# Kernel optimization log

Measured on AMD Instinct MI355X. Metric: run time of the kernel, lower is better.

## Reference

```python
import jax, jax.numpy as jnp
import numpy as np

EMBED_DIM = 2048
NUM_HEADS = 32
HEAD_DIM = EMBED_DIM // NUM_HEADS  # 64
SCALE = HEAD_DIM ** -0.5


def setup_inputs() -> dict:
    key = jax.random.key(0)
    k1, k2, k3, k4, k5 = jax.random.split(key, 5)
    B, S, D = 1, 2048, EMBED_DIM
    return {
        "hidden_states": jax.random.normal(k1, (B, S, D), jnp.float32),
        "w_qkv": jax.random.normal(k2, (3 * D, D), jnp.float32) * (D ** -0.5),
        "b_qkv": jax.random.normal(k3, (3 * D,), jnp.float32) * 0.02,
        "w_out": jax.random.normal(k4, (D, D), jnp.float32) * (D ** -0.5),
        "b_out": jax.random.normal(k5, (D,), jnp.float32) * 0.02,
    }


def reference(hidden_states, w_qkv, b_qkv, w_out, b_out):
    B, S, D = hidden_states.shape
    H, Hd = NUM_HEADS, HEAD_DIM
    # fused QKV projection: [B,S,3D]
    qkv = jnp.einsum("bsd,ed->bse", hidden_states, w_qkv) + b_qkv
    q, k, v = jnp.split(qkv, 3, axis=-1)
    # [B,H,S,Hd]
    q = q.reshape(B, S, H, Hd).transpose(0, 2, 1, 3)
    k = k.reshape(B, S, H, Hd).transpose(0, 2, 1, 3)
    v = v.reshape(B, S, H, Hd).transpose(0, 2, 1, 3)
    scores = jnp.einsum("bhqd,bhkd->bhqk", q, k) * SCALE
    causal = jnp.tril(jnp.ones((S, S), bool))  # [S,S]
    scores = jnp.where(causal, scores, jnp.finfo(scores.dtype).min)
    probs = jax.nn.softmax(scores, axis=-1)
    attn = jnp.einsum("bhqk,bhkd->bhqd", probs, v)
    attn = attn.transpose(0, 2, 1, 3).reshape(B, S, D)
    return jnp.einsum("bsd,ed->bse", attn, w_out) + b_out
```

## Files before the change

### kernel.cpp

```cpp
#include <hip/hip_runtime.h>
#include <hip/hip_bf16.h>

typedef __bf16 bf16;
typedef __attribute__((ext_vector_type(8))) __bf16 bf16x8;
typedef __attribute__((ext_vector_type(4))) float f32x4;

#define S_LEN 2048
#define DM 2048
#define NH 32
#define HD 64
#define QKV_LD 6144
#define SCALE2 0.18033688011112042f
#define DEFER_THR 8.0f

__device__ __forceinline__ float fast_exp2(float x) {
  return __builtin_amdgcn_exp2f(x);
}

__device__ __forceinline__ void gload_lds16(const bf16* g, const bf16* l) {
  __builtin_amdgcn_global_load_lds(
      (const __attribute__((address_space(1))) void*)(uintptr_t)g,
      (__attribute__((address_space(3))) void*)(uint32_t)(uintptr_t)l,
      16, 0, 0);
}

template <int CTRL>
__device__ __forceinline__ float fdpp(float x) {
  return __builtin_bit_cast(float,
      __builtin_amdgcn_update_dpp(0, __builtin_bit_cast(int, x), CTRL, 0xF, 0xF, true));
}
__device__ __forceinline__ float red16_max(float x) {
  x = fmaxf(x, fdpp<0xB1>(x));
  x = fmaxf(x, fdpp<0x4E>(x));
  x = fmaxf(x, fdpp<0x141>(x));
  x = fmaxf(x, fdpp<0x140>(x));
  return x;
}

__global__ __launch_bounds__(256) void cvt3_f32_bf16(
    const float* __restrict__ s0, bf16* __restrict__ d0, const int n0,
    const float* __restrict__ s1, bf16* __restrict__ d1, const int n1,
    const float* __restrict__ s2, bf16* __restrict__ d2, const int n2)
{
  const int total = n0 + n1 + n2;
  const int stride = gridDim.x * blockDim.x;
  for (int i = blockIdx.x * blockDim.x + threadIdx.x; i < total; i += stride) {
    const float* s; bf16* d; int j = i;
    if (j < n0)            { s = s0; d = d0; }
    else if (j - n0 < n1)  { s = s1; d = d1; j -= n0; }
    else                   { s = s2; d = d2; j -= n0 + n1; }
    const f32x4 a = *(const f32x4*)(s + (size_t)j * 8);
    const f32x4 b = *(const f32x4*)(s + (size_t)j * 8 + 4);
    bf16x8 r;
    r[0] = (bf16)a[0]; r[1] = (bf16)a[1]; r[2] = (bf16)a[2]; r[3] = (bf16)a[3];
    r[4] = (bf16)b[0]; r[5] = (bf16)b[1]; r[6] = (bf16)b[2]; r[7] = (bf16)b[3];
    *(bf16x8*)(d + (size_t)j * 8) = r;
  }
}

template <int BM, int BN, int WRN, int WCN, int NT, int MINW, typename TO>
__global__ __launch_bounds__(NT, MINW) void gemm_pipe(
    const bf16* __restrict__ A, const bf16* __restrict__ W,
    const float* __restrict__ bias, TO* __restrict__ C,
    const int M, const int N, const int K)
{
  constexpr int WM = BM / WRN, WN = BN / WCN;
  constexpr int MI = WM / 16, NI = WN / 16;
  constexpr int CA = (BM * 64 * 2) / (NT * 16);
  constexpr int CB = (BN * 64 * 2) / (NT * 16);
  constexpr int BUFE = (BM + BN) * 64;
  __shared__ __align__(16) bf16 lds[2 * BUFE];
  const int tid  = threadIdx.x;
  const int lane = tid & 63;
  const int wid  = tid >> 6;
  const int wr = wid / WCN, wc = wid % WCN;
  const int row0 = blockIdx.y * BM, col0 = blockIdx.x * BN;
  const int lq = lane & 15, seg = lane >> 4;

  const f32x4 fz = {0.f, 0.f, 0.f, 0.f};
  f32x4 acc[MI][NI];
#pragma unroll
  for (int i = 0; i < MI; ++i)
#pragma unroll
    for (int j = 0; j < NI; ++j) acc[i][j] = fz;

  auto stage = [&](const int kt, const int b) {
    const int k0 = kt << 6;
    bf16* Ab = lds + b * BUFE;
    bf16* Bb = Ab + BM * 64;
#pragma unroll
    for (int c = 0; c < CA; ++c) {
      const int off16 = c * NT + tid;
      const int row = off16 >> 3;
      const int ch  = (off16 & 7) ^ (row & 7);
      gload_lds16(A + (size_t)(row0 + row) * K + k0 + (ch << 3),
                  Ab + (size_t)(c * NT + (wid << 6)) * 8);
    }
#pragma unroll
    for (int c = 0; c < CB; ++c) {
      const int off16 = c * NT + tid;
      const int row = off16 >> 3;
      const int ch  = (off16 & 7) ^ (row & 7);
      gload_lds16(W + (size_t)(col0 + row) * K + k0 + (ch << 3),
                  Bb + (size_t)(c * NT + (wid << 6)) * 8);
    }
  };

  const int nt = K >> 6;
  stage(0, 0);

  for (int t = 0; t < nt; ++t) {
    asm volatile("s_waitcnt vmcnt(0)" ::: "memory");
    __builtin_amdgcn_s_barrier();
    asm volatile("" ::: "memory");
    if (t + 1 < nt) stage(t + 1, (t + 1) & 1);

    const bf16* Ab = lds + (t & 1) * BUFE;
    const bf16* Bb = Ab + BM * 64;
#pragma unroll
    for (int kk = 0; kk < 2; ++kk) {
      bf16x8 af[MI], bfr[NI];
#pragma unroll
      for (int i = 0; i < MI; ++i) {
        const int row = wr * WM + (i << 4) + lq;
        af[i] = *(const bf16x8*)(Ab + row * 64 +
                 ((((kk << 2) + seg) ^ (row & 7)) << 3));
      }
#pragma unroll
      for (int j = 0; j < NI; ++j) {
        const int row = wc * WN + (j << 4) + lq;
        bfr[j] = *(const bf16x8*)(Bb + row * 64 +
                 ((((kk << 2) + seg) ^ (row & 7)) << 3));
      }
      __builtin_amdgcn_s_setprio(1);
#pragma unroll
      for (int i = 0; i < MI; ++i)
#pragma unroll
        for (int j = 0; j < NI; ++j)
          acc[i][j] = __builtin_amdgcn_mfma_f32_16x16x32_bf16(af[i], bfr[j], acc[i][j], 0, 0, 0);
      __builtin_amdgcn_s_setprio(0);
    }
  }

#pragma unroll
  for (int j = 0; j < NI; ++j) {
    const int col = col0 + wc * WN + (j << 4) + lq;
    const float bv = bias[col];
#pragma unroll
    for (int i = 0; i < MI; ++i) {
      const int rbase = row0 + wr * WM + (i << 4) + (seg << 2);
#pragma unroll
      for (int r = 0; r < 4; ++r)
        C[(size_t)(rbase + r) * N + col] = (TO)(acc[i][j][r] + bv);
    }
  }
}

struct QTile {
  bf16x8 qf[2];
  f32x4  o[4];
  f32x4  ls;
  float  m;
};

__device__ __forceinline__ void qtile_init(QTile& st, const bf16* Qg,
                                           const int lq, const int seg) {
  const bf16x8 r0 = *(const bf16x8*)(Qg + (size_t)lq * QKV_LD + seg * 8);
  const bf16x8 r1 = *(const bf16x8*)(Qg + (size_t)lq * QKV_LD + 32 + seg * 8);
#pragma unroll
  for (int j = 0; j < 8; ++j) {
    st.qf[0][j] = (bf16)((float)r0[j] * SCALE2);
    st.qf[1][j] = (bf16)((float)r1[j] * SCALE2);
  }
  const f32x4 fz = {0.f, 0.f, 0.f, 0.f};
#pragma unroll
  for (int r = 0; r < 4; ++r) st.o[r] = fz;
  st.ls = fz;
  st.m = -1e30f;
}

__device__ __forceinline__ void qtile_step(
    QTile& st, const int qb, const int nt,
    const int ws, const int lq, const int seg,
    const bf16 (&Ks)[64][64], const bf16 (&Vt)[64][64], bf16 (&Psw)[16][64])
{
  const f32x4 fz = {0.f, 0.f, 0.f, 0.f};
  f32x4 s[4];
  __builtin_amdgcn_s_setprio(1);
#pragma unroll
  for (int ct = 0; ct < 4; ++ct) {
    s[ct] = fz;
#pragma unroll
    for (int ks = 0; ks < 2; ++ks) {
      const int blk = ((ks << 2) + seg) ^ (lq & 7);
      const bf16x8 kf = *(const bf16x8*)(&Ks[(ct << 4) + lq][blk << 3]);
      s[ct] = __builtin_amdgcn_mfma_f32_16x16x32_bf16(st.qf[ks], kf, s[ct], 0, 0, 0);
    }
  }
  __builtin_amdgcn_s_setprio(0);

  if (nt == qb) {
#pragma unroll
    for (int ct = 0; ct < 4; ++ct) {
      const int key = (nt << 6) + (ct << 4) + lq;
#pragma unroll
      for (int r = 0; r < 4; ++r) {
        const int qrow = (qb << 6) + (ws << 4) + (seg << 2) + r;
        if (key > qrow) s[ct][r] = -1e30f;
      }
    }
  }

  float tm = s[0][0];
#pragma unroll
  for (int ct = 0; ct < 4; ++ct)
#pragma unroll
    for (int r = 0; r < 4; ++r) tm = fmaxf(tm, s[ct][r]);
  tm = red16_max(tm);
  if (tm > st.m + DEFER_THR) {
    const float sc = fast_exp2(st.m - tm);
    st.m = tm;
    st.ls *= sc;
#pragma unroll
    for (int dt = 0; dt < 4; ++dt) st.o[dt] *= sc;
  }

#pragma unroll
  for (int ct = 0; ct < 4; ++ct)
#pragma unroll
    for (int r = 0; r < 4; ++r) {
      const int q = (seg << 2) + r;
      const int colp = ((ct << 4) + lq) ^ ((q & 7) << 3);
      Psw[q][colp] = (bf16)fast_exp2(s[ct][r] - st.m);
    }

  bf16x8 ones;
#pragma unroll
  for (int j = 0; j < 8; ++j) ones[j] = (bf16)1.0f;
  __builtin_amdgcn_s_setprio(1);
#pragma unroll
  for (int ks = 0; ks < 2; ++ks) {
    const int blkp = ((ks << 2) + seg) ^ (lq & 7);
    const bf16x8 af = *(const bf16x8*)(&Psw[lq][blkp << 3]);
    st.ls = __builtin_amdgcn_mfma_f32_16x16x32_bf16(af, ones, st.ls, 0, 0, 0);
#pragma unroll
    for (int dt = 0; dt < 4; ++dt) {
      const int xv = (lq & 7) ^ (((dt << 1) + (lq >> 3)) & 7);
      const int blkv = ((ks << 2) + seg) ^ xv;
      const bf16x8 bv = *(const bf16x8*)(&Vt[(dt << 4) + lq][blkv << 3]);
      st.o[dt] = __builtin_amdgcn_mfma_f32_16x16x32_bf16(af, bv, st.o[dt], 0, 0, 0);
    }
  }
  __builtin_amdgcn_s_setprio(0);
}

__device__ __forceinline__ void qtile_store(
    const QTile& st, bf16* __restrict__ out, const int qb, const int h,
    const int ws, const int lq, const int seg)
{
  float rinv[4];
#pragma unroll
  for (int r = 0; r < 4; ++r) rinv[r] = 1.f / st.ls[r];
#pragma unroll
  for (int dt = 0; dt < 4; ++dt)
#pragma unroll
    for (int r = 0; r < 4; ++r) {
      const int qrow = (qb << 6) + (ws << 4) + (seg << 2) + r;
      out[(size_t)qrow * DM + h * HD + (dt << 4) + lq] =
          (bf16)(st.o[dt][r] * rinv[r]);
    }
}

__global__ __launch_bounds__(512, 4) void attn_flash(
    const bf16* __restrict__ qkv, bf16* __restrict__ out)
{
  __shared__ __align__(16) bf16 Ks[2][64][64];
  __shared__ __align__(16) bf16 Vt[2][64][64];
  __shared__ __align__(16) bf16 Ps[8][16][64];
  const int bid = blockIdx.x;
  const int xcd = bid & 7, idx = bid >> 3;
  const int h   = (xcd << 2) | (idx >> 4);
  const int qbA = idx & 15;
  const int qbB = 31 - qbA;
  const int tid = threadIdx.x;
  const int lane = tid & 63, wid = tid >> 6;
  const int lq = lane & 15, seg = lane >> 4;
  const int myqb = (wid < 4) ? qbA : qbB;
  const int ws   = wid & 3;

  const bf16* Kg = qkv + DM + h * HD;
  const bf16* Vg = qkv + 2 * DM + h * HD;

  QTile st;
  qtile_init(st, qkv + (size_t)(myqb * 64 + ws * 16) * QKV_LD + h * HD, lq, seg);

  const int srow = tid >> 3, sch = tid & 7;

  {
    const bf16x8 k0 = *(const bf16x8*)(Kg + (size_t)srow * QKV_LD + (sch << 3));
    const bf16x8 v0 = *(const bf16x8*)(Vg + (size_t)srow * QKV_LD + (sch << 3));
    *(bf16x8*)(&Ks[0][srow][(sch ^ (srow & 7)) << 3]) = k0;
#pragma unroll
    for (int j = 0; j < 8; ++j)
      Vt[0][(sch << 3) + j][srow ^ ((j ^ sch) << 3)] = v0[j];
  }
  __syncthreads();

  for (int nt = 0; nt <= qbB; ++nt) {
    bf16x8 kr, vr;
    if (nt < qbB) {
      const int row = ((nt + 1) << 6) + srow;
      kr = *(const bf16x8*)(Kg + (size_t)row * QKV_LD + (sch << 3));
      vr = *(const bf16x8*)(Vg + (size_t)row * QKV_LD + (sch << 3));
    }

    if (nt <= myqb)
      qtile_step(st, myqb, nt, ws, lq, seg, Ks[nt & 1], Vt[nt & 1], Ps[wid]);

    if (nt < qbB) {
      const int b = (nt + 1) & 1;
      *(bf16x8*)(&Ks[b][srow][(sch ^ (srow & 7)) << 3]) = kr;
#pragma unroll
      for (int j = 0; j < 8; ++j)
        Vt[b][(sch << 3) + j][srow ^ ((j ^ sch) << 3)] = vr[j];
    }
    __syncthreads();
  }

  qtile_store(st, out, myqb, h, ws, lq, seg);
}

extern "C" void kernel_launch(void* const* d_in, const int* in_sizes, int n_in,
                              void* d_out, int out_size, void* d_ws, size_t ws_size,
                              hipStream_t stream) {
  (void)in_sizes; (void)n_in; (void)out_size; (void)ws_size;
  const float* hidden = (const float*)d_in[0];
  const float* w_qkv  = (const float*)d_in[1];
  const float* b_qkv  = (const float*)d_in[2];
  const float* w_out  = (const float*)d_in[3];
  const float* b_out  = (const float*)d_in[4];
  float* out = (float*)d_out;

  bf16* qkvbuf  = (bf16*)d_ws;
  bf16* attnbuf = qkvbuf  + (size_t)S_LEN * (3 * DM);
  bf16* hidb    = attnbuf + (size_t)S_LEN * DM;
  bf16* wqkvb   = hidb    + (size_t)S_LEN * DM;
  bf16* woutb   = wqkvb   + (size_t)(3 * DM) * DM;

  dim3 blk(256);
  cvt3_f32_bf16<<<dim3(2048), blk, 0, stream>>>(
      hidden, hidb, (S_LEN * DM) / 8,
      w_qkv, wqkvb, (3 * DM * DM) / 8,
      w_out, woutb, (DM * DM) / 8);
  gemm_pipe<128, 192, 2, 4, 512, 2, bf16><<<dim3(32, 16), dim3(512), 0, stream>>>(
      hidb, wqkvb, b_qkv, qkvbuf, S_LEN, 3 * DM, DM);
  attn_flash<<<dim3(512), dim3(512), 0, stream>>>(qkvbuf, attnbuf);
  gemm_pipe<64, 128, 1, 4, 256, 2, float><<<dim3(16, 32), dim3(256), 0, stream>>>(
      attnbuf, woutb, b_out, out, S_LEN, DM, DM);
}
```

Measured before the change: 141.5 us.

## Process two 64-key tiles per barrier iteration in flash attention

The attention loop now stages 128 keys (two 64-row K/V tiles) per double-buffered stage and computes both score tiles before a single max/rescale step. This halves the number of __syncthreads barriers and online-softmax rescale decisions, and gives the scheduler more independent MFMA work per iteration. In exchange, LDS use doubles and the launch bound drops from 4 to 2 blocks per CU, which may reduce occupancy and latency hiding.

Result: slower. 154.4 us (+9.1%).

```diff
diff --git a/kernel.cpp b/kernel.cpp
--- a/kernel.cpp
+++ b/kernel.cpp
@@ -179,43 +179,102 @@
   st.m = -1e30f;
 }
 
-__device__ __forceinline__ void qtile_step(
-    QTile& st, const int qb, const int nt,
+__device__ __forceinline__ void pv_sub(
+    QTile& st, const f32x4 (&s)[4], const int lq, const int seg,
+    const bf16 (&Vt)[64][64], bf16 (&Psw)[16][64])
+{
+#pragma unroll
+  for (int ct = 0; ct < 4; ++ct)
+#pragma unroll
+    for (int r = 0; r < 4; ++r) {
+      const int q = (seg << 2) + r;
+      const int colp = ((ct << 4) + lq) ^ ((q & 7) << 3);
+      Psw[q][colp] = (bf16)fast_exp2(s[ct][r] - st.m);
+    }
+  bf16x8 ones;
+#pragma unroll
+  for (int j = 0; j < 8; ++j) ones[j] = (bf16)1.0f;
+  __builtin_amdgcn_s_setprio(1);
+#pragma unroll
+  for (int ks = 0; ks < 2; ++ks) {
+    const int blkp = ((ks << 2) + seg) ^ (lq & 7);
+    const bf16x8 af = *(const bf16x8*)(&Psw[lq][blkp << 3]);
+    st.ls = __builtin_amdgcn_mfma_f32_16x16x32_bf16(af, ones, st.ls, 0, 0, 0);
+#pragma unroll
+    for (int dt = 0; dt < 4; ++dt) {
+      const int xv = (lq & 7) ^ (((dt << 1) + (lq >> 3)) & 7);
+      const int blkv = ((ks << 2) + seg) ^ xv;
+      const bf16x8 bv = *(const bf16x8*)(&Vt[(dt << 4) + lq][blkv << 3]);
+      st.o[dt] = __builtin_amdgcn_mfma_f32_16x16x32_bf16(af, bv, st.o[dt], 0, 0, 0);
+    }
+  }
+  __builtin_amdgcn_s_setprio(0);
+}
+
+__device__ __forceinline__ void qtile_step2(
+    QTile& st, const int qb, const int nt0, const bool do1,
     const int ws, const int lq, const int seg,
-    const bf16 (&Ks)[64][64], const bf16 (&Vt)[64][64], bf16 (&Psw)[16][64])
+    const bf16 (&Ks2)[2][64][64], const bf16 (&Vt2)[2][64][64],
+    bf16 (&Psw)[16][64])
 {
   const f32x4 fz = {0.f, 0.f, 0.f, 0.f};
-  f32x4 s[4];
+  f32x4 s0[4], s1[4];
   __builtin_amdgcn_s_setprio(1);
 #pragma unroll
   for (int ct = 0; ct < 4; ++ct) {
-    s[ct] = fz;
+    s0[ct] = fz;
 #pragma unroll
     for (int ks = 0; ks < 2; ++ks) {
       const int blk = ((ks << 2) + seg) ^ (lq & 7);
-      const bf16x8 kf = *(const bf16x8*)(&Ks[(ct << 4) + lq][blk << 3]);
-      s[ct] = __builtin_amdgcn_mfma_f32_16x16x32_bf16(st.qf[ks], kf, s[ct], 0, 0, 0);
+      const bf16x8 kf = *(const bf16x8*)(&Ks2[0][(ct << 4) + lq][blk << 3]);
+      s0[ct] = __builtin_amdgcn_mfma_f32_16x16x32_bf16(st.qf[ks], kf, s0[ct], 0, 0, 0);
+    }
+  }
+  if (do1) {
+#pragma unroll
+    for (int ct = 0; ct < 4; ++ct) {
+      s1[ct] = fz;
+#pragma unroll
+      for (int ks = 0; ks < 2; ++ks) {
+        const int blk = ((ks << 2) + seg) ^ (lq & 7);
+        const bf16x8 kf = *(const bf16x8*)(&Ks2[1][(ct << 4) + lq][blk << 3]);
+        s1[ct] = __builtin_amdgcn_mfma_f32_16x16x32_bf16(st.qf[ks], kf, s1[ct], 0, 0, 0);
+      }
     }
   }
   __builtin_amdgcn_s_setprio(0);
 
-  if (nt == qb) {
+  const int qrow0 = (qb << 6) + (ws << 4) + (seg << 2);
+  if (nt0 == qb) {
 #pragma unroll
     for (int ct = 0; ct < 4; ++ct) {
-      const int key = (nt << 6) + (ct << 4) + lq;
-#pragma unroll
-      for (int r = 0; r < 4; ++r) {
-        const int qrow = (qb << 6) + (ws << 4) + (seg << 2) + r;
-        if (key > qrow) s[ct][r] = -1e30f;
-      }
-    }
-  }
-
-  float tm = s[0][0];
+      const int key = (nt0 << 6) + (ct << 4) + lq;
+#pragma unroll
+      for (int r = 0; r < 4; ++r)
+        if (key > qrow0 + r) s0[ct][r] = -1e30f;
+    }
+  }
+  if (do1 && nt0 + 1 == qb) {
+#pragma unroll
+    for (int ct = 0; ct < 4; ++ct) {
+      const int key = ((nt0 + 1) << 6) + (ct << 4) + lq;
+#pragma unroll
+      for (int r = 0; r < 4; ++r)
+        if (key > qrow0 + r) s1[ct][r] = -1e30f;
+    }
+  }
+
+  float tm = s0[0][0];
 #pragma unroll
   for (int ct = 0; ct < 4; ++ct)
 #pragma unroll
-    for (int r = 0; r < 4; ++r) tm = fmaxf(tm, s[ct][r]);
+    for (int r = 0; r < 4; ++r) tm = fmaxf(tm, s0[ct][r]);
+  if (do1) {
+#pragma unroll
+    for (int ct = 0; ct < 4; ++ct)
+#pragma unroll
+      for (int r = 0; r < 4; ++r) tm = fmaxf(tm, s1[ct][r]);
+  }
   tm = red16_max(tm);
   if (tm > st.m + DEFER_THR) {
     const float sc = fast_exp2(st.m - tm);
@@ -225,33 +284,8 @@
     for (int dt = 0; dt < 4; ++dt) st.o[dt] *= sc;
   }
 
-#pragma unroll
-  for (int ct = 0; ct < 4; ++ct)
-#pragma unroll
-    for (int r = 0; r < 4; ++r) {
-      const int q = (seg << 2) + r;
-      const int colp = ((ct << 4) + lq) ^ ((q & 7) << 3);
-      Psw[q][colp] = (bf16)fast_exp2(s[ct][r] - st.m);
-    }
-
-  bf16x8 ones;
-#pragma unroll
-  for (int j = 0; j < 8; ++j) ones[j] = (bf16)1.0f;
-  __builtin_amdgcn_s_setprio(1);
-#pragma unroll
-  for (int ks = 0; ks < 2; ++ks) {
-    const int blkp = ((ks << 2) + seg) ^ (lq & 7);
-    const bf16x8 af = *(const bf16x8*)(&Psw[lq][blkp << 3]);
-    st.ls = __builtin_amdgcn_mfma_f32_16x16x32_bf16(af, ones, st.ls, 0, 0, 0);
-#pragma unroll
-    for (int dt = 0; dt < 4; ++dt) {
-      const int xv = (lq & 7) ^ (((dt << 1) + (lq >> 3)) & 7);
-      const int blkv = ((ks << 2) + seg) ^ xv;
-      const bf16x8 bv = *(const bf16x8*)(&Vt[(dt << 4) + lq][blkv << 3]);
-      st.o[dt] = __builtin_amdgcn_mfma_f32_16x16x32_bf16(af, bv, st.o[dt], 0, 0, 0);
-    }
-  }
-  __builtin_amdgcn_s_setprio(0);
+  pv_sub(st, s0, lq, seg, Vt2[0], Psw);
+  if (do1) pv_sub(st, s1, lq, seg, Vt2[1], Psw);
 }
 
 __device__ __forceinline__ void qtile_store(
@@ -271,11 +305,11 @@
     }
 }
 
-__global__ __launch_bounds__(512, 4) void attn_flash(
+__global__ __launch_bounds__(512, 2) void attn_flash(
     const bf16* __restrict__ qkv, bf16* __restrict__ out)
 {
-  __shared__ __align__(16) bf16 Ks[2][64][64];
-  __shared__ __align__(16) bf16 Vt[2][64][64];
+  __shared__ __align__(16) bf16 Ks[2][2][64][64];
+  __shared__ __align__(16) bf16 Vt[2][2][64][64];
   __shared__ __align__(16) bf16 Ps[8][16][64];
   const int bid = blockIdx.x;
   const int xcd = bid & 7, idx = bid >> 3;
@@ -296,33 +330,44 @@
 
   const int srow = tid >> 3, sch = tid & 7;
 
-  {
-    const bf16x8 k0 = *(const bf16x8*)(Kg + (size_t)srow * QKV_LD + (sch << 3));
-    const bf16x8 v0 = *(const bf16x8*)(Vg + (size_t)srow * QKV_LD + (sch << 3));
-    *(bf16x8*)(&Ks[0][srow][(sch ^ (srow & 7)) << 3]) = k0;
+#pragma unroll
+  for (int c = 0; c < 2; ++c) {
+    const int row = (c << 6) + srow;
+    const bf16x8 k0 = *(const bf16x8*)(Kg + (size_t)row * QKV_LD + (sch << 3));
+    const bf16x8 v0 = *(const bf16x8*)(Vg + (size_t)row * QKV_LD + (sch << 3));
+    *(bf16x8*)(&Ks[0][c][srow][(sch ^ (srow & 7)) << 3]) = k0;
 #pragma unroll
     for (int j = 0; j < 8; ++j)
-      Vt[0][(sch << 3) + j][srow ^ ((j ^ sch) << 3)] = v0[j];
+      Vt[0][c][(sch << 3) + j][srow ^ ((j ^ sch) << 3)] = v0[j];
   }
   __syncthreads();
 
-  for (int nt = 0; nt <= qbB; ++nt) {
-    bf16x8 kr, vr;
-    if (nt < qbB) {
-      const int row = ((nt + 1) << 6) + srow;
-      kr = *(const bf16x8*)(Kg + (size_t)row * QKV_LD + (sch << 3));
-      vr = *(const bf16x8*)(Vg + (size_t)row * QKV_LD + (sch << 3));
-    }
-
-    if (nt <= myqb)
-      qtile_step(st, myqb, nt, ws, lq, seg, Ks[nt & 1], Vt[nt & 1], Ps[wid]);
-
-    if (nt < qbB) {
-      const int b = (nt + 1) & 1;
-      *(bf16x8*)(&Ks[b][srow][(sch ^ (srow & 7)) << 3]) = kr;
-#pragma unroll
-      for (int j = 0; j < 8; ++j)
-        Vt[b][(sch << 3) + j][srow ^ ((j ^ sch) << 3)] = vr[j];
+  const int nsup = (qbB >> 1) + 1;
+  for (int T = 0; T < nsup; ++T) {
+    bf16x8 kr[2], vr[2];
+    if (T + 1 < nsup) {
+#pragma unroll
+      for (int c = 0; c < 2; ++c) {
+        const int row = ((T + 1) << 7) + (c << 6) + srow;
+        kr[c] = *(const bf16x8*)(Kg + (size_t)row * QKV_LD + (sch << 3));
+        vr[c] = *(const bf16x8*)(Vg + (size_t)row * QKV_LD + (sch << 3));
+      }
+    }
+
+    const int nt0 = T << 1;
+    if (nt0 <= myqb)
+      qtile_step2(st, myqb, nt0, (nt0 + 1) <= myqb, ws, lq, seg,
+                  Ks[T & 1], Vt[T & 1], Ps[wid]);
+
+    if (T + 1 < nsup) {
+      const int b = (T + 1) & 1;
+#pragma unroll
+      for (int c = 0; c < 2; ++c) {
+        *(bf16x8*)(&Ks[b][c][srow][(sch ^ (srow & 7)) << 3]) = kr[c];
+#pragma unroll
+        for (int j = 0; j < 8; ++j)
+          Vt[b][c][(sch << 3) + j][srow ^ ((j ^ sch) << 3)] = vr[c][j];
+      }
     }
     __syncthreads();
   }
```

## Fuse fp32-to-bf16 weight conversion into GEMM tile loading

Applied to the files above, without the earlier changes.

Drops the standalone weight conversion pass and has both projection GEMMs load fp32 weights directly, converting them to bf16 in registers before writing to LDS. Activation tiles still use async global-to-LDS loads. This removes the separate read and write of the full weight matrices. In exchange, every row-block re-reads fp32 weights at twice the bytes, and B tiles go through registers with a plain __syncthreads pipeline.

Measured after the change: 143.7 us. Within noise of the previous version (+1.6%).

```diff
diff --git a/kernel.cpp b/kernel.cpp
--- a/kernel.cpp
+++ b/kernel.cpp
@@ -37,57 +37,99 @@
   return x;
 }
 
-__global__ __launch_bounds__(256) void cvt3_f32_bf16(
-    const float* __restrict__ s0, bf16* __restrict__ d0, const int n0,
-    const float* __restrict__ s1, bf16* __restrict__ d1, const int n1,
-    const float* __restrict__ s2, bf16* __restrict__ d2, const int n2)
-{
-  const int total = n0 + n1 + n2;
+__global__ __launch_bounds__(256) void cvt_f32_bf16(
+    const float* __restrict__ src, bf16* __restrict__ dst, const int n8)
+{
   const int stride = gridDim.x * blockDim.x;
-  for (int i = blockIdx.x * blockDim.x + threadIdx.x; i < total; i += stride) {
-    const float* s; bf16* d; int j = i;
-    if (j < n0)            { s = s0; d = d0; }
-    else if (j - n0 < n1)  { s = s1; d = d1; j -= n0; }
-    else                   { s = s2; d = d2; j -= n0 + n1; }
-    const f32x4 a = *(const f32x4*)(s + (size_t)j * 8);
-    const f32x4 b = *(const f32x4*)(s + (size_t)j * 8 + 4);
+  for (int i = blockIdx.x * blockDim.x + threadIdx.x; i < n8; i += stride) {
+    const f32x4 a = *(const f32x4*)(src + (size_t)i * 8);
+    const f32x4 b = *(const f32x4*)(src + (size_t)i * 8 + 4);
     bf16x8 r;
     r[0] = (bf16)a[0]; r[1] = (bf16)a[1]; r[2] = (bf16)a[2]; r[3] = (bf16)a[3];
     r[4] = (bf16)b[0]; r[5] = (bf16)b[1]; r[6] = (bf16)b[2]; r[7] = (bf16)b[3];
-    *(bf16x8*)(d + (size_t)j * 8) = r;
+    *(bf16x8*)(dst + (size_t)i * 8) = r;
+  }
+}
+
+template <int BM, int BN, int WRN, int WCN, typename TO>
+__device__ __forceinline__ void gemm_compute_tile(
+    const bf16* __restrict__ Ab, f32x4 (*acc)[BN / WCN / 16],
+    const int wr, const int wc, const int lq, const int seg)
+{
+  constexpr int WM = BM / WRN, WN = BN / WCN;
+  constexpr int MI = WM / 16, NI = WN / 16;
+  const bf16* Bb = Ab + BM * 64;
+#pragma unroll
+  for (int kk = 0; kk < 2; ++kk) {
+    bf16x8 af[MI], bfr[NI];
+#pragma unroll
+    for (int i = 0; i < MI; ++i) {
+      const int row = wr * WM + (i << 4) + lq;
+      af[i] = *(const bf16x8*)(Ab + row * 64 +
+               ((((kk << 2) + seg) ^ (row & 7)) << 3));
+    }
+#pragma unroll
+    for (int j = 0; j < NI; ++j) {
+      const int row = wc * WN + (j << 4) + lq;
+      bfr[j] = *(const bf16x8*)(Bb + row * 64 +
+               ((((kk << 2) + seg) ^ (row & 7)) << 3));
+    }
+    __builtin_amdgcn_s_setprio(1);
+#pragma unroll
+    for (int i = 0; i < MI; ++i)
+#pragma unroll
+      for (int j = 0; j < NI; ++j)
+        acc[i][j] = __builtin_amdgcn_mfma_f32_16x16x32_bf16(af[i], bfr[j], acc[i][j], 0, 0, 0);
+    __builtin_amdgcn_s_setprio(0);
+  }
+}
+
+template <int BM, int BN, int WRN, int WCN, typename TO>
+__device__ __forceinline__ void gemm_epilogue(
+    f32x4 (*acc)[BN / WCN / 16], const float* __restrict__ bias,
+    TO* __restrict__ C, const int N, const int row0, const int col0,
+    const int wr, const int wc, const int lq, const int seg)
+{
+  constexpr int WM = BM / WRN, WN = BN / WCN;
+  constexpr int MI = WM / 16, NI = WN / 16;
+#pragma unroll
+  for (int j = 0; j < NI; ++j) {
+    const int col = col0 + wc * WN + (j << 4) + lq;
+    const float bv = bias[col];
+#pragma unroll
+    for (int i = 0; i < MI; ++i) {
+      const int rbase = row0 + wr * WM + (i << 4) + (seg << 2);
+#pragma unroll
+      for (int r = 0; r < 4; ++r)
+        C[(size_t)(rbase + r) * N + col] = (TO)(acc[i][j][r] + bv);
+    }
   }
 }
 
 template <int BM, int BN, int WRN, int WCN, int NT, int MINW, typename TO>
-__global__ __launch_bounds__(NT, MINW) void gemm_pipe(
-    const bf16* __restrict__ A, const bf16* __restrict__ W,
+__global__ __launch_bounds__(NT, MINW) void gemm_mix(
+    const bf16* __restrict__ A, const float* __restrict__ Wf,
     const float* __restrict__ bias, TO* __restrict__ C,
     const int M, const int N, const int K)
 {
-  constexpr int WM = BM / WRN, WN = BN / WCN;
-  constexpr int MI = WM / 16, NI = WN / 16;
   constexpr int CA = (BM * 64 * 2) / (NT * 16);
   constexpr int CB = (BN * 64 * 2) / (NT * 16);
   constexpr int BUFE = (BM + BN) * 64;
   __shared__ __align__(16) bf16 lds[2 * BUFE];
-  const int tid  = threadIdx.x;
-  const int lane = tid & 63;
-  const int wid  = tid >> 6;
+  const int tid = threadIdx.x, lane = tid & 63, wid = tid >> 6;
   const int wr = wid / WCN, wc = wid % WCN;
   const int row0 = blockIdx.y * BM, col0 = blockIdx.x * BN;
   const int lq = lane & 15, seg = lane >> 4;
 
   const f32x4 fz = {0.f, 0.f, 0.f, 0.f};
-  f32x4 acc[MI][NI];
-#pragma unroll
-  for (int i = 0; i < MI; ++i)
-#pragma unroll
-    for (int j = 0; j < NI; ++j) acc[i][j] = fz;
-
-  auto stage = [&](const int kt, const int b) {
+  f32x4 acc[BM / WRN / 16][BN / WCN / 16];
+#pragma unroll
+  for (int i = 0; i < BM / WRN / 16; ++i)
+#pragma unroll
+    for (int j = 0; j < BN / WCN / 16; ++j) acc[i][j] = fz;
+
+  auto stageA = [&](const int kt, bf16* Ab) {
     const int k0 = kt << 6;
-    bf16* Ab = lds + b * BUFE;
-    bf16* Bb = Ab + BM * 64;
 #pragma unroll
     for (int c = 0; c < CA; ++c) {
       const int off16 = c * NT + tid;
@@ -96,64 +138,56 @@
       gload_lds16(A + (size_t)(row0 + row) * K + k0 + (ch << 3),
                   Ab + (size_t)(c * NT + (wid << 6)) * 8);
     }
+  };
+  auto loadW = [&](const int kt, f32x4 (&w)[CB][2]) {
+    const int k0 = kt << 6;
 #pragma unroll
     for (int c = 0; c < CB; ++c) {
       const int off16 = c * NT + tid;
       const int row = off16 >> 3;
       const int ch  = (off16 & 7) ^ (row & 7);
-      gload_lds16(W + (size_t)(col0 + row) * K + k0 + (ch << 3),
-                  Bb + (size_t)(c * NT + (wid << 6)) * 8);
+      const float* p = Wf + (size_t)(col0 + row) * K + k0 + (ch << 3);
+      w[c][0] = *(const f32x4*)p;
+      w[c][1] = *(const f32x4*)(p + 4);
     }
   };
+  auto writeW = [&](bf16* Bb, const f32x4 (&w)[CB][2]) {
+#pragma unroll
+    for (int c = 0; c < CB; ++c) {
+      bf16x8 r;
+#pragma unroll
+      for (int j = 0; j < 4; ++j) {
+        r[j]     = (bf16)w[c][0][j];
+        r[4 + j] = (bf16)w[c][1][j];
+      }
+      *(bf16x8*)(Bb + (size_t)(c * NT + tid) * 8) = r;
+    }
+  };
 
   const int nt = K >> 6;
-  stage(0, 0);
+  {
+    f32x4 w0[CB][2];
+    stageA(0, lds);
+    loadW(0, w0);
+    writeW(lds + BM * 64, w0);
+  }
+  __syncthreads();
 
   for (int t = 0; t < nt; ++t) {
-    asm volatile("s_waitcnt vmcnt(0)" ::: "memory");
-    __builtin_amdgcn_s_barrier();
-    asm volatile("" ::: "memory");
-    if (t + 1 < nt) stage(t + 1, (t + 1) & 1);
-
-    const bf16* Ab = lds + (t & 1) * BUFE;
-    const bf16* Bb = Ab + BM * 64;
-#pragma unroll
-    for (int kk = 0; kk < 2; ++kk) {
-      bf16x8 af[MI], bfr[NI];
-#pragma unroll
-      for (int i = 0; i < MI; ++i) {
-        const int row = wr * WM + (i << 4) + lq;
-        af[i] = *(const bf16x8*)(Ab + row * 64 +
-                 ((((kk << 2) + seg) ^ (row & 7)) << 3));
-      }
-#pragma unroll
-      for (int j = 0; j < NI; ++j) {
-        const int row = wc * WN + (j << 4) + lq;
-        bfr[j] = *(const bf16x8*)(Bb + row * 64 +
-                 ((((kk << 2) + seg) ^ (row & 7)) << 3));
-      }
-      __builtin_amdgcn_s_setprio(1);
-#pragma unroll
-      for (int i = 0; i < MI; ++i)
-#pragma unroll
-        for (int j = 0; j < NI; ++j)
-          acc[i][j] = __builtin_amdgcn_mfma_f32_16x16x32_bf16(af[i], bfr[j], acc[i][j], 0, 0, 0);
-      __builtin_amdgcn_s_setprio(0);
-    }
-  }
-
-#pragma unroll
-  for (int j = 0; j < NI; ++j) {
-    const int col = col0 + wc * WN + (j << 4) + lq;
-    const float bv = bias[col];
-#pragma unroll
-    for (int i = 0; i < MI; ++i) {
-      const int rbase = row0 + wr * WM + (i << 4) + (seg << 2);
-#pragma unroll
-      for (int r = 0; r < 4; ++r)
-        C[(size_t)(rbase + r) * N + col] = (TO)(acc[i][j][r] + bv);
-    }
-  }
+    f32x4 wn[CB][2];
+    const bool more = (t + 1 < nt);
+    if (more) {
+      stageA(t + 1, lds + ((t + 1) & 1) * BUFE);
+      loadW(t + 1, wn);
+    }
+    gemm_compute_tile<BM, BN, WRN, WCN, TO>(lds + (t & 1) * BUFE, acc,
+                                            wr, wc, lq, seg);
+    if (more)
+      writeW(lds + ((t + 1) & 1) * BUFE + BM * 64, wn);
+    __syncthreads();
+  }
+  gemm_epilogue<BM, BN, WRN, WCN, TO>(acc, bias, C, N, row0, col0,
+                                      wr, wc, lq, seg);
 }
 
 struct QTile {
@@ -344,17 +378,12 @@
   bf16* qkvbuf  = (bf16*)d_ws;
   bf16* attnbuf = qkvbuf  + (size_t)S_LEN * (3 * DM);
   bf16* hidb    = attnbuf + (size_t)S_LEN * DM;
-  bf16* wqkvb   = hidb    + (size_t)S_LEN * DM;
-  bf16* woutb   = wqkvb   + (size_t)(3 * DM) * DM;
 
   dim3 blk(256);
-  cvt3_f32_bf16<<<dim3(2048), blk, 0, stream>>>(
-      hidden, hidb, (S_LEN * DM) / 8,
-      w_qkv, wqkvb, (3 * DM * DM) / 8,
-      w_out, woutb, (DM * DM) / 8);
-  gemm_pipe<128, 192, 2, 4, 512, 2, bf16><<<dim3(32, 16), dim3(512), 0, stream>>>(
-      hidb, wqkvb, b_qkv, qkvbuf, S_LEN, 3 * DM, DM);
+  cvt_f32_bf16<<<dim3(2048), blk, 0, stream>>>(hidden, hidb, (S_LEN * DM) / 8);
+  gemm_mix<128, 192, 2, 4, 512, 2, bf16><<<dim3(32, 16), dim3(512), 0, stream>>>(
+      hidb, w_qkv, b_qkv, qkvbuf, S_LEN, 3 * DM, DM);
   attn_flash<<<dim3(512), dim3(512), 0, stream>>>(qkvbuf, attnbuf);
-  gemm_pipe<64, 128, 1, 4, 256, 2, float><<<dim3(16, 32), dim3(256), 0, stream>>>(
-      attnbuf, woutb, b_out, out, S_LEN, DM, DM);
-}
+  gemm_mix<64, 128, 1, 4, 256, 2, float><<<dim3(16, 32), dim3(256), 0, stream>>>(
+      attnbuf, w_out, b_out, out, S_LEN, DM, DM);
+}
```
